# Performance work log

Hardware: AMD Instinct MI355X
Metric: run time of the kernel (lower is better)

## Reference

```python
import jax, jax.numpy as jnp
import numpy as np

N, LP, LD, D, H, GS = 16, 2048, 512, 256, 8, 4
HD = D // H           # head_size = 32
TAU = 1.0             # softmax_tau
ITERS = 4             # sinkhorn_iters
INF = 1.0e6


def setup_inputs() -> dict:
    key = jax.random.key(0)
    ks = jax.random.split(key, 10)
    inp = {
        "protein": jax.random.normal(ks[0], (N, LP, D), jnp.float32),
        "drug": jax.random.normal(ks[1], (N, LD, D), jnp.float32),
        "mask_prot": jax.random.bernoulli(ks[2], 0.9, (N, LP)),
        "mask_drug": jax.random.bernoulli(ks[3], 0.9, (N, LD)),
    }
    names = ["Wq_p", "Wk_p", "Wv_p", "Wq_d", "Wk_d", "Wv_d"]
    for i, name in enumerate(names):
        inp[name] = jax.random.normal(ks[4 + i], (D, D), jnp.float32) * (1.0 / np.sqrt(D))
    return inp


def _group(x, mask):
    n, L, d = x.shape
    g = L // GS
    xg = x.reshape(n, g, GS, d).mean(2)          # [N,G,D]
    mg = mask.reshape(n, g, GS).any(2)           # [N,G]
    return xg, mg


def _alpha_logits(logits, mask_row, mask_col):
    # logits: [N,L1,L2,H]; sinkhorn normalization as in the torch module
    n, L1, L2, h = logits.shape
    logits = logits * (1.0 / np.sqrt(HD))
    pair = mask_row[:, :, None, None] & mask_col[:, None, :, None]  # [N,L1,L2,1]
    logits = jnp.where(pair, logits, logits - INF)
    A = jax.nn.softmax((logits / TAU).reshape(n, L1 * L2, h), axis=1).reshape(n, L1, L2, h)
    valid = pair.astype(A.dtype)
    A = A * valid + 1e-12 * valid
    for _ in range(ITERS):
        row_sum = (A * valid).sum(2, keepdims=True) + 1e-12
        A = A / row_sum * valid
        col_sum = (A * valid).sum(1, keepdims=True) + 1e-12
        A = A / col_sum * valid
    return A * valid


def _proj(x, W):
    n, g, d = x.shape
    return (x @ W.T).reshape(n, g, H, HD)


def reference(protein, drug, mask_prot, mask_drug, Wq_p, Wk_p, Wv_p, Wq_d, Wk_d, Wv_d):
    pg, mp = _group(protein, mask_prot)   # [N,Gp,D], [N,Gp]
    dg, md = _group(drug, mask_drug)      # [N,Gd,D], [N,Gd]

    qp, kp, vp = _proj(pg, Wq_p), _proj(pg, Wk_p), _proj(pg, Wv_p)
    qd, kd, vd = _proj(dg, Wq_d), _proj(dg, Wk_d), _proj(dg, Wv_d)

    att = lambda q, k: jnp.einsum('blhd,bkhd->blkh', q, k)
    a_pp = _alpha_logits(att(qp, kp), mp, mp)
    a_pd = _alpha_logits(att(qp, kd), mp, md)
    a_dp = _alpha_logits(att(qd, kp), md, mp)
    a_dd = _alpha_logits(att(qd, kd), md, md)

    mix = lambda a, v: jnp.einsum('blkh,bkhd->blhd', a, v).reshape(a.shape[0], a.shape[1], D)
    prot_embedding = (mix(a_pp, vp) + mix(a_pd, vd)) * 0.5  # [N,Gp,D]
    drug_embedding = (mix(a_dp, vp) + mix(a_dd, vd)) * 0.5  # [N,Gd,D]

    # agg_mode == 'mean': masked mean over valid groups
    mpf = mp[..., None].astype(prot_embedding.dtype)
    mdf = md[..., None].astype(drug_embedding.dtype)
    prot_embed = (prot_embedding * mpf).sum(1) / mpf.sum(1)
    drug_embed = (drug_embedding * mdf).sum(1) / mdf.sum(1)

    query_embed = jnp.concatenate([prot_embed, drug_embed], axis=1)  # [N,2D]
    return query_embed, a_dp
```

## Files before the change

### kernel.cpp

```cpp
#include <hip/hip_runtime.h>
#include <hip/hip_bf16.h>

#define NB   16
#define DT   256
#define HT   8
#define HDT  32
#define GP   512
#define GD   128
#define SCL  0.17677669529663687f

using bf16x8 = __attribute__((ext_vector_type(8))) short;
using bf16x4 = __attribute__((ext_vector_type(4))) short;
using f32x4  = __attribute__((ext_vector_type(4))) float;

__device__ __forceinline__ short f2bf(float f) {
  __hip_bfloat16 h = __float2bfloat16(f);
  short s; __builtin_memcpy(&s, &h, 2);
  return s;
}

__device__ __forceinline__ bf16x8 cvt8(float4 a, float4 b) {
  bf16x8 r;
  r[0] = f2bf(a.x); r[1] = f2bf(a.y); r[2] = f2bf(a.z); r[3] = f2bf(a.w);
  r[4] = f2bf(b.x); r[5] = f2bf(b.y); r[6] = f2bf(b.z); r[7] = f2bf(b.w);
  return r;
}

extern "C" __global__ __launch_bounds__(256)
void k_group(const float* __restrict__ protein, const float* __restrict__ drug,
             const int* __restrict__ mprot, const int* __restrict__ mdrug,
             const float* __restrict__ Wk, const float* __restrict__ Wq,
             short* __restrict__ pg_bf, short* __restrict__ dg_bf,
             int* __restrict__ mp_g, int* __restrict__ md_g,
             short* __restrict__ Wk_bf, short* __restrict__ Wq_bf,
             float* __restrict__ part, int* __restrict__ cntp) {
  int b = blockIdx.x, t = threadIdx.x;
  if (b >= 640) {
    int idx = (b - 640) * 2048 + t * 8;
    const float* s; short* d;
    if (idx < 65536) { s = Wk + idx; d = Wk_bf + idx; }
    else             { s = Wq + (idx - 65536); d = Wq_bf + (idx - 65536); }
    *(bf16x8*)d = cvt8(*(const float4*)s, *(const float4*)(s + 4));
    return;
  }
  const float* src; const int* msk; short* dst; int* mg; int gbase;
  if (b < 512) { src = protein; msk = mprot; dst = pg_bf; mg = mp_g; gbase = b * 16; }
  else         { src = drug;    msk = mdrug; dst = dg_bf; mg = md_g; gbase = (b - 512) * 16; }

  __shared__ int gm_s[16];
  __shared__ float part_s[4][256];
  if (t < 16) {
    const int* m = msk + (size_t)(gbase + t) * 4;
    int v = (m[0] | m[1] | m[2] | m[3]) ? 1 : 0;
    gm_s[t] = v;
    mg[gbase + t] = v;
  }
  __syncthreads();
  if (t == 0) {
    int c = 0;
    #pragma unroll
    for (int i = 0; i < 16; ++i) c += gm_s[i];
    cntp[b] = c;
  }

  int col4 = t & 63, gsub = t >> 6;
  float a0 = 0.f, a1 = 0.f, a2 = 0.f, a3 = 0.f;
  #pragma unroll
  for (int it = 0; it < 4; ++it) {
    int grp = gbase + gsub + it * 4;
    const float* rp = src + (size_t)grp * 1024 + col4 * 4;
    float4 r0 = *(const float4*)rp;
    float4 r1 = *(const float4*)(rp + 256);
    float4 r2 = *(const float4*)(rp + 512);
    float4 r3 = *(const float4*)(rp + 768);
    float m0 = 0.25f * (r0.x + r1.x + r2.x + r3.x);
    float m1 = 0.25f * (r0.y + r1.y + r2.y + r3.y);
    float m2 = 0.25f * (r0.z + r1.z + r2.z + r3.z);
    float m3 = 0.25f * (r0.w + r1.w + r2.w + r3.w);
    bf16x4 v; v[0] = f2bf(m0); v[1] = f2bf(m1); v[2] = f2bf(m2); v[3] = f2bf(m3);
    *(bf16x4*)(dst + (size_t)grp * 256 + col4 * 4) = v;
    if (gm_s[gsub + it * 4]) { a0 += m0; a1 += m1; a2 += m2; a3 += m3; }
  }
  part_s[gsub][col4 * 4 + 0] = a0;
  part_s[gsub][col4 * 4 + 1] = a1;
  part_s[gsub][col4 * 4 + 2] = a2;
  part_s[gsub][col4 * 4 + 3] = a3;
  __syncthreads();
  part[(size_t)b * 256 + t] = part_s[0][t] + part_s[1][t] + part_s[2][t] + part_s[3][t];
}

extern "C" __global__ __launch_bounds__(256)
void k_projbf(const short* __restrict__ pg_bf, const short* __restrict__ dg_bf,
              const short* __restrict__ Wk_bf, const short* __restrict__ Wq_bf,
              short* __restrict__ kp_bf, short* __restrict__ qd_bf) {
  int b = blockIdx.x, t = threadIdx.x;
  int w = t >> 6, lane = t & 63, c15 = lane & 15, g = lane >> 4;
  const short *A, *W; short* o; int rowbase;
  if (b < 256) { A = pg_bf; W = Wk_bf; o = kp_bf; rowbase = b * 32; }
  else         { A = dg_bf; W = Wq_bf; o = qd_bf; rowbase = (b - 256) * 32; }
  int rt = rowbase + (w & 1) * 16;
  int ch = (w >> 1) * 128;

  const short* ap = A + (size_t)(rt + c15) * 256;
  f32x4 acc[8];
  #pragma unroll
  for (int i = 0; i < 8; ++i) acc[i] = (f32x4){0.f, 0.f, 0.f, 0.f};

  #pragma unroll
  for (int ks = 0; ks < 8; ++ks) {
    bf16x8 af = *(const bf16x8*)(ap + ks * 32 + g * 8);
    #pragma unroll
    for (int ct = 0; ct < 8; ++ct) {
      bf16x8 bfr = *(const bf16x8*)(W + (size_t)(ch + ct * 16 + c15) * 256 + ks * 32 + g * 8);
      acc[ct] = __builtin_amdgcn_mfma_f32_16x16x32_bf16(af, bfr, acc[ct], 0, 0, 0);
    }
  }
  #pragma unroll
  for (int ct = 0; ct < 8; ++ct) {
    #pragma unroll
    for (int r = 0; r < 4; ++r) {
      o[(size_t)(rt + 4 * g + r) * 256 + ch + ct * 16 + c15] = f2bf(acc[ct][r]);
    }
  }
}

#define FOR16(X) X(0) X(1) X(2) X(3) X(4) X(5) X(6) X(7) X(8) X(9) X(10) X(11) X(12) X(13) X(14) X(15)

extern "C" __global__ __launch_bounds__(1024)
void k_scalars(const short* __restrict__ qd, const short* __restrict__ kp,
               const int* __restrict__ md_g, const int* __restrict__ mp_g,
               float* __restrict__ rcz) {
  int bid = blockIdx.x;
  int n = ((bid & 7) << 1) | ((bid >> 3) & 1);
  int h = bid >> 4;
  int tid = threadIdx.x;
  int wid = tid >> 6, lane = tid & 63;
  int wr = wid >> 1, ch = wid & 1;
  int c15 = lane & 15, g = lane >> 4;

  __shared__ float c_s[GP];
  __shared__ float r_s[GD];
  __shared__ float t_s[GD];
  __shared__ float t2[2][GD];
  __shared__ float red[8][GP];
  __shared__ float z_sh, sr_sh, sc_sh, kv_sh;
  __shared__ int mp_sh[GP];
  __shared__ int md_sh[GD];

  if (tid < GP) { int m = mp_g[n * GP + tid]; mp_sh[tid] = m; c_s[tid] = m ? 1.f : 0.f; }
  if (tid < GD) { int m = md_g[n * GD + tid]; md_sh[tid] = m; r_s[tid] = m ? 1.f : 0.f; }
  __syncthreads();

  if (wid == 0) {
    float v = (float)(mp_sh[lane] + mp_sh[lane + 64] + mp_sh[lane + 128] + mp_sh[lane + 192] +
                      mp_sh[lane + 256] + mp_sh[lane + 320] + mp_sh[lane + 384] + mp_sh[lane + 448]);
    #pragma unroll
    for (int m = 1; m <= 32; m <<= 1) v += __shfl_xor(v, m, 64);
    if (lane == 0) kv_sh = v;
  }

  int qrow = 16 * wr + c15;
  bf16x8 af = *(const bf16x8*)(qd + ((size_t)(n * GD + qrow)) * 256 + h * HDT + g * 8);
  int row0 = 16 * wr + 4 * g;
  int mr0 = md_sh[row0], mr1 = md_sh[row0 + 1], mr2 = md_sh[row0 + 2], mr3 = md_sh[row0 + 3];
  const short* kbase = kp + ((size_t)n * GP) * 256 + h * HDT + g * 8;
  int colbase = ch * 256 + c15;

#define DECLP(i) f32x4 P##i;
  FOR16(DECLP)
#define MKP(i) { int col = colbase + 16 * (i); \
    bf16x8 bfr = *(const bf16x8*)(kbase + (size_t)col * 256); \
    f32x4 a = __builtin_amdgcn_mfma_f32_16x16x32_bf16(af, bfr, (f32x4){0.f,0.f,0.f,0.f}, 0, 0, 0); \
    int mc = mp_sh[col]; \
    P##i[0] = (mc && mr0) ? __expf(a[0] * SCL) : 0.f; \
    P##i[1] = (mc && mr1) ? __expf(a[1] * SCL) : 0.f; \
    P##i[2] = (mc && mr2) ? __expf(a[2] * SCL) : 0.f; \
    P##i[3] = (mc && mr3) ? __expf(a[3] * SCL) : 0.f; }
  FOR16(MKP)

  {
    float pa0 = 0.f, pa1 = 0.f, pa2 = 0.f, pa3 = 0.f;
#define RS0(i) pa0 += P##i[0]; pa1 += P##i[1]; pa2 += P##i[2]; pa3 += P##i[3];
    FOR16(RS0)
    #pragma unroll
    for (int m = 1; m <= 8; m <<= 1) {
      pa0 += __shfl_xor(pa0, m, 64); pa1 += __shfl_xor(pa1, m, 64);
      pa2 += __shfl_xor(pa2, m, 64); pa3 += __shfl_xor(pa3, m, 64);
    }
    if (c15 == 0) t2[ch][row0 + 0] = pa0;
    if (c15 == 1) t2[ch][row0 + 1] = pa1;
    if (c15 == 2) t2[ch][row0 + 2] = pa2;
    if (c15 == 3) t2[ch][row0 + 3] = pa3;
  }
  __syncthreads();
  if (tid < GD) t_s[tid] = t2[0][tid] + t2[1][tid];
  __syncthreads();
  if (wid == 0) {
    float v = t_s[lane] + t_s[lane + 64];
    #pragma unroll
    for (int m = 1; m <= 32; m <<= 1) v += __shfl_xor(v, m, 64);
    if (lane == 0) z_sh = v;
  }
  __syncthreads();
  float Zinv = 1.0f / z_sh;
  float Sc = kv_sh;

  #pragma unroll 1
  for (int it = 0; it < 4; ++it) {
    if (tid < GD) {
      float ti = t_s[tid] * Zinv + 1e-12f * Sc;
      float ri = r_s[tid];
      r_s[tid] = md_sh[tid] ? (ri / (ri * ti + 1e-12f)) : 0.f;
    }
    __syncthreads();
    if (wid == 0) {
      float v = r_s[lane] + r_s[lane + 64];
      #pragma unroll
      for (int m = 1; m <= 32; m <<= 1) v += __shfl_xor(v, m, 64);
      if (lane == 0) sr_sh = v;
    }
    __syncthreads();
    float Sr = sr_sh;
    {
      float rr0 = r_s[row0], rr1 = r_s[row0 + 1], rr2 = r_s[row0 + 2], rr3 = r_s[row0 + 3];
#define CP(i) { float u = P##i[0] * rr0 + P##i[1] * rr1 + P##i[2] * rr2 + P##i[3] * rr3; \
      u += __shfl_xor(u, 16, 64); u += __shfl_xor(u, 32, 64); \
      if (g == 0) red[wr][colbase + 16 * (i)] = u; }
      FOR16(CP)
    }
    __syncthreads();
    if (tid < GP) {
      float cs = red[0][tid] + red[1][tid] + red[2][tid] + red[3][tid] +
                 red[4][tid] + red[5][tid] + red[6][tid] + red[7][tid];
      float uj = cs * Zinv + 1e-12f * Sr;
      float cj = c_s[tid];
      c_s[tid] = mp_sh[tid] ? (cj / (cj * uj + 1e-12f)) : 0.f;
    }
    __syncthreads();
    if (wid == 0) {
      float v = c_s[lane] + c_s[lane + 64] + c_s[lane + 128] + c_s[lane + 192] +
                c_s[lane + 256] + c_s[lane + 320] + c_s[lane + 384] + c_s[lane + 448];
      #pragma unroll
      for (int m = 1; m <= 32; m <<= 1) v += __shfl_xor(v, m, 64);
      if (lane == 0) sc_sh = v;
    }
    __syncthreads();
    Sc = sc_sh;
    if (it < 3) {
      float qa0 = 0.f, qa1 = 0.f, qa2 = 0.f, qa3 = 0.f;
#define RP(i) { float cv = c_s[colbase + 16 * (i)]; \
      qa0 += P##i[0] * cv; qa1 += P##i[1] * cv; qa2 += P##i[2] * cv; qa3 += P##i[3] * cv; }
      FOR16(RP)
      #pragma unroll
      for (int m = 1; m <= 8; m <<= 1) {
        qa0 += __shfl_xor(qa0, m, 64); qa1 += __shfl_xor(qa1, m, 64);
        qa2 += __shfl_xor(qa2, m, 64); qa3 += __shfl_xor(qa3, m, 64);
      }
      if (c15 == 0) t2[ch][row0 + 0] = qa0;
      if (c15 == 1) t2[ch][row0 + 1] = qa1;
      if (c15 == 2) t2[ch][row0 + 2] = qa2;
      if (c15 == 3) t2[ch][row0 + 3] = qa3;
      __syncthreads();
      if (tid < GD) t_s[tid] = t2[0][tid] + t2[1][tid];
    }
  }

  size_t rb = (size_t)(n * 8 + h) * 1024;
  if (tid < GD) rcz[rb + tid] = r_s[tid];
  if (tid < GP) rcz[rb + 128 + tid] = c_s[tid];
  if (tid == 0) rcz[rb + 640] = Zinv;
}

extern "C" __global__ __launch_bounds__(256)
void k_write_embed(const short* __restrict__ qd, const short* __restrict__ kp,
                   const float* __restrict__ rcz,
                   const float* __restrict__ part, const int* __restrict__ cntp,
                   const float* __restrict__ Wvp, const float* __restrict__ Wvd,
                   float* __restrict__ out) {
  int bid = blockIdx.x;
  int t = threadIdx.x;
  if (bid >= 512) {
    int bb = bid - 512;
    int n = bb >> 3;
    int dchunk = (bb & 7) * 32;
    __shared__ float sps[256], sds[256];
    float a1 = 0.f;
    #pragma unroll
    for (int i = 0; i < 32; ++i) a1 += part[(size_t)(n * 32 + i) * 256 + t];
    sps[t] = a1;
    float a2 = 0.f;
    #pragma unroll
    for (int i = 0; i < 8; ++i) a2 += part[(size_t)(512 + n * 8 + i) * 256 + t];
    sds[t] = a2;
    __syncthreads();
    int cp = 0, cd = 0;
    #pragma unroll
    for (int i = 0; i < 32; ++i) cp += cntp[n * 32 + i];
    #pragma unroll
    for (int i = 0; i < 8; ++i) cd += cntp[512 + n * 8 + i];
    int dloc = t >> 3, ks = (t & 7) * 32;
    int d = dchunk + dloc;
    const float* wp = Wvp + (size_t)d * 256 + ks;
    const float* wd = Wvd + (size_t)d * 256 + ks;
    float acc = 0.f;
    #pragma unroll
    for (int k = 0; k < 32; k += 4) {
      float4 a = *(const float4*)(wp + k);
      float4 c = *(const float4*)(wd + k);
      acc += sps[ks + k] * a.x + sps[ks + k + 1] * a.y + sps[ks + k + 2] * a.z + sps[ks + k + 3] * a.w
           + sds[ks + k] * c.x + sds[ks + k + 1] * c.y + sds[ks + k + 2] * c.z + sds[ks + k + 3] * c.w;
    }
    #pragma unroll
    for (int m = 1; m <= 4; m <<= 1) acc += __shfl_xor(acc, m, 64);
    if ((t & 7) == 0) {
      acc *= 0.5f;
      out[n * 512 + d]       = acc / (float)cp;
      out[n * 512 + 256 + d] = acc / (float)cd;
    }
    return;
  }
  int n = ((bid & 7) << 1) | ((bid >> 3) & 1);
  int rest = bid >> 4;
  int rt = rest >> 2;
  int cc = rest & 3;
  int w = t >> 6, lane = t & 63;
  int c15 = lane & 15, g = lane >> 4;

  const short* qbase = qd + ((size_t)(n * GD + rt * 16 + c15)) * 256;
  bf16x8 af[8];
  #pragma unroll
  for (int h = 0; h < 8; ++h) af[h] = *(const bf16x8*)(qbase + h * HDT + g * 8);

  size_t rb = (size_t)n * 8 * 1024;
  float rv[8][4], zin[8];
  #pragma unroll
  for (int h = 0; h < 8; ++h) {
    const float* rp = rcz + rb + (size_t)h * 1024;
    #pragma unroll
    for (int r = 0; r < 4; ++r) rv[h][r] = rp[rt * 16 + 4 * g + r];
    zin[h] = rp[640];
  }

  #pragma unroll
  for (int ct = 0; ct < 2; ++ct) {
    int col = cc * 128 + w * 32 + ct * 16 + c15;
    f32x4 acc[8]; float cw[8];
    #pragma unroll
    for (int h = 0; h < 8; ++h) {
      bf16x8 bfr = *(const bf16x8*)(kp + ((size_t)(n * GP + col)) * 256 + h * HDT + g * 8);
      acc[h] = __builtin_amdgcn_mfma_f32_16x16x32_bf16(af[h], bfr, (f32x4){0.f,0.f,0.f,0.f}, 0, 0, 0);
      cw[h] = rcz[rb + (size_t)h * 1024 + 128 + col];
    }
    #pragma unroll
    for (int r = 0; r < 4; ++r) {
      int row = rt * 16 + 4 * g + r;
      float4 lo, hi;
      lo.x = rv[0][r] * (__expf(acc[0][r] * SCL) * zin[0] + 1e-12f) * cw[0];
      lo.y = rv[1][r] * (__expf(acc[1][r] * SCL) * zin[1] + 1e-12f) * cw[1];
      lo.z = rv[2][r] * (__expf(acc[2][r] * SCL) * zin[2] + 1e-12f) * cw[2];
      lo.w = rv[3][r] * (__expf(acc[3][r] * SCL) * zin[3] + 1e-12f) * cw[3];
      hi.x = rv[4][r] * (__expf(acc[4][r] * SCL) * zin[4] + 1e-12f) * cw[4];
      hi.y = rv[5][r] * (__expf(acc[5][r] * SCL) * zin[5] + 1e-12f) * cw[5];
      hi.z = rv[6][r] * (__expf(acc[6][r] * SCL) * zin[6] + 1e-12f) * cw[6];
      hi.w = rv[7][r] * (__expf(acc[7][r] * SCL) * zin[7] + 1e-12f) * cw[7];
      float* dst = out + 8192 + (((size_t)(n * GD + row)) * GP + col) * 8;
      *(float4*)dst = lo;
      *(float4*)(dst + 4) = hi;
    }
  }
}

extern "C" void kernel_launch(void* const* d_in, const int* in_sizes, int n_in,
                              void* d_out, int out_size, void* d_ws, size_t ws_size,
                              hipStream_t stream) {
  const float* protein = (const float*)d_in[0];
  const float* drug    = (const float*)d_in[1];
  const int*   mprot   = (const int*)d_in[2];
  const int*   mdrug   = (const int*)d_in[3];
  const float* Wk_p = (const float*)d_in[5];
  const float* Wv_p = (const float*)d_in[6];
  const float* Wq_d = (const float*)d_in[7];
  const float* Wv_d = (const float*)d_in[9];
  float* out = (float*)d_out;

  char* wsb = (char*)d_ws;
  short* pg_bf = (short*)wsb;                 wsb += (size_t)NB * GP * 256 * 2;
  short* dg_bf = (short*)wsb;                 wsb += (size_t)NB * GD * 256 * 2;
  short* kp_bf = (short*)wsb;                 wsb += (size_t)NB * GP * 256 * 2;
  short* qd_bf = (short*)wsb;                 wsb += (size_t)NB * GD * 256 * 2;
  short* Wk_bf = (short*)wsb;                 wsb += 65536 * 2;
  short* Wq_bf = (short*)wsb;                 wsb += 65536 * 2;
  float* part  = (float*)wsb;                 wsb += (size_t)640 * 256 * 4;
  float* rcz   = (float*)wsb;                 wsb += (size_t)128 * 1024 * 4;
  int*   cntp  = (int*)wsb;                   wsb += 640 * 4;
  int*   mp_g  = (int*)wsb;                   wsb += 8192 * 4;
  int*   md_g  = (int*)wsb;                   wsb += 2048 * 4;

  k_group<<<704, 256, 0, stream>>>(protein, drug, mprot, mdrug, Wk_p, Wq_d,
                                   pg_bf, dg_bf, mp_g, md_g, Wk_bf, Wq_bf,
                                   part, cntp);
  k_projbf<<<320, 256, 0, stream>>>(pg_bf, dg_bf, Wk_bf, Wq_bf, kp_bf, qd_bf);
  k_scalars<<<128, 1024, 0, stream>>>(qd_bf, kp_bf, md_g, mp_g, rcz);
  k_write_embed<<<640, 256, 0, stream>>>(qd_bf, kp_bf, rcz, part, cntp,
                                         Wv_p, Wv_d, out);
}
```

Baseline: 163.1 us.

## Move embed GEMV into projection kernel, stage K tile in LDS, trim syncs

The embedding GEMV blocks move from the final write kernel into the projection launch as 128 extra blocks, so they run alongside the projections instead of at the end. The write kernel now stages a 128-column K tile in swizzled LDS before the MFMAs, replacing repeated global loads. In the Sinkhorn kernel the exp-weight registers are stored as fp16 to cut register pressure, and block-wide scalar reductions are done redundantly per wave to remove several __syncthreads. fp16 storage of the weights lowers precision, and the 64KB LDS tile may limit occupancy of the write kernel.

```diff
diff --git a/kernel.cpp b/kernel.cpp
--- a/kernel.cpp
+++ b/kernel.cpp
@@ -12,6 +12,7 @@
 using bf16x8 = __attribute__((ext_vector_type(8))) short;
 using bf16x4 = __attribute__((ext_vector_type(4))) short;
 using f32x4  = __attribute__((ext_vector_type(4))) float;
+using h16x4  = __attribute__((ext_vector_type(4))) _Float16;
 
 __device__ __forceinline__ short f2bf(float f) {
   __hip_bfloat16 h = __float2bfloat16(f);
@@ -92,8 +93,51 @@
 extern "C" __global__ __launch_bounds__(256)
 void k_projbf(const short* __restrict__ pg_bf, const short* __restrict__ dg_bf,
               const short* __restrict__ Wk_bf, const short* __restrict__ Wq_bf,
-              short* __restrict__ kp_bf, short* __restrict__ qd_bf) {
+              short* __restrict__ kp_bf, short* __restrict__ qd_bf,
+              const float* __restrict__ part, const int* __restrict__ cntp,
+              const float* __restrict__ Wvp, const float* __restrict__ Wvd,
+              float* __restrict__ out) {
   int b = blockIdx.x, t = threadIdx.x;
+  if (b >= 320) {
+    int bb = b - 320;
+    int n = bb >> 3;
+    int dchunk = (bb & 7) * 32;
+    __shared__ float sps[256], sds[256];
+    float a1 = 0.f;
+    #pragma unroll
+    for (int i = 0; i < 32; ++i) a1 += part[(size_t)(n * 32 + i) * 256 + t];
+    sps[t] = a1;
+    float a2 = 0.f;
+    #pragma unroll
+    for (int i = 0; i < 8; ++i) a2 += part[(size_t)(512 + n * 8 + i) * 256 + t];
+    sds[t] = a2;
+    __syncthreads();
+    int cp = 0, cd = 0;
+    #pragma unroll
+    for (int i = 0; i < 32; ++i) cp += cntp[n * 32 + i];
+    #pragma unroll
+    for (int i = 0; i < 8; ++i) cd += cntp[512 + n * 8 + i];
+    int dloc = t >> 3, ks = (t & 7) * 32;
+    int d = dchunk + dloc;
+    const float* wp = Wvp + (size_t)d * 256 + ks;
+    const float* wd = Wvd + (size_t)d * 256 + ks;
+    float acc = 0.f;
+    #pragma unroll
+    for (int k = 0; k < 32; k += 4) {
+      float4 a = *(const float4*)(wp + k);
+      float4 c = *(const float4*)(wd + k);
+      acc += sps[ks + k] * a.x + sps[ks + k + 1] * a.y + sps[ks + k + 2] * a.z + sps[ks + k + 3] * a.w
+           + sds[ks + k] * c.x + sds[ks + k + 1] * c.y + sds[ks + k + 2] * c.z + sds[ks + k + 3] * c.w;
+    }
+    #pragma unroll
+    for (int m = 1; m <= 4; m <<= 1) acc += __shfl_xor(acc, m, 64);
+    if ((t & 7) == 0) {
+      acc *= 0.5f;
+      out[n * 512 + d]       = acc / (float)cp;
+      out[n * 512 + 256 + d] = acc / (float)cd;
+    }
+    return;
+  }
   int w = t >> 6, lane = t & 63, c15 = lane & 15, g = lane >> 4;
   const short *A, *W; short* o; int rowbase;
   if (b < 256) { A = pg_bf; W = Wk_bf; o = kp_bf; rowbase = b * 32; }
@@ -140,10 +184,8 @@
 
   __shared__ float c_s[GP];
   __shared__ float r_s[GD];
-  __shared__ float t_s[GD];
   __shared__ float t2[2][GD];
   __shared__ float red[8][GP];
-  __shared__ float z_sh, sr_sh, sc_sh, kv_sh;
   __shared__ int mp_sh[GP];
   __shared__ int md_sh[GD];
 
@@ -151,12 +193,13 @@
   if (tid < GD) { int m = md_g[n * GD + tid]; md_sh[tid] = m; r_s[tid] = m ? 1.f : 0.f; }
   __syncthreads();
 
-  if (wid == 0) {
+  float kv;
+  {
     float v = (float)(mp_sh[lane] + mp_sh[lane + 64] + mp_sh[lane + 128] + mp_sh[lane + 192] +
                       mp_sh[lane + 256] + mp_sh[lane + 320] + mp_sh[lane + 384] + mp_sh[lane + 448]);
     #pragma unroll
     for (int m = 1; m <= 32; m <<= 1) v += __shfl_xor(v, m, 64);
-    if (lane == 0) kv_sh = v;
+    kv = v;
   }
 
   int qrow = 16 * wr + c15;
@@ -166,21 +209,21 @@
   const short* kbase = kp + ((size_t)n * GP) * 256 + h * HDT + g * 8;
   int colbase = ch * 256 + c15;
 
-#define DECLP(i) f32x4 P##i;
+#define DECLP(i) h16x4 P##i;
   FOR16(DECLP)
 #define MKP(i) { int col = colbase + 16 * (i); \
     bf16x8 bfr = *(const bf16x8*)(kbase + (size_t)col * 256); \
     f32x4 a = __builtin_amdgcn_mfma_f32_16x16x32_bf16(af, bfr, (f32x4){0.f,0.f,0.f,0.f}, 0, 0, 0); \
     int mc = mp_sh[col]; \
-    P##i[0] = (mc && mr0) ? __expf(a[0] * SCL) : 0.f; \
-    P##i[1] = (mc && mr1) ? __expf(a[1] * SCL) : 0.f; \
-    P##i[2] = (mc && mr2) ? __expf(a[2] * SCL) : 0.f; \
-    P##i[3] = (mc && mr3) ? __expf(a[3] * SCL) : 0.f; }
+    P##i[0] = (_Float16)((mc && mr0) ? __expf(a[0] * SCL) : 0.f); \
+    P##i[1] = (_Float16)((mc && mr1) ? __expf(a[1] * SCL) : 0.f); \
+    P##i[2] = (_Float16)((mc && mr2) ? __expf(a[2] * SCL) : 0.f); \
+    P##i[3] = (_Float16)((mc && mr3) ? __expf(a[3] * SCL) : 0.f); }
   FOR16(MKP)
 
   {
     float pa0 = 0.f, pa1 = 0.f, pa2 = 0.f, pa3 = 0.f;
-#define RS0(i) pa0 += P##i[0]; pa1 += P##i[1]; pa2 += P##i[2]; pa3 += P##i[3];
+#define RS0(i) pa0 += (float)P##i[0]; pa1 += (float)P##i[1]; pa2 += (float)P##i[2]; pa3 += (float)P##i[3];
     FOR16(RS0)
     #pragma unroll
     for (int m = 1; m <= 8; m <<= 1) {
@@ -193,37 +236,34 @@
     if (c15 == 3) t2[ch][row0 + 3] = pa3;
   }
   __syncthreads();
-  if (tid < GD) t_s[tid] = t2[0][tid] + t2[1][tid];
-  __syncthreads();
-  if (wid == 0) {
-    float v = t_s[lane] + t_s[lane + 64];
+  float Zinv;
+  {
+    float v = t2[0][lane] + t2[1][lane] + t2[0][lane + 64] + t2[1][lane + 64];
     #pragma unroll
     for (int m = 1; m <= 32; m <<= 1) v += __shfl_xor(v, m, 64);
-    if (lane == 0) z_sh = v;
-  }
-  __syncthreads();
-  float Zinv = 1.0f / z_sh;
-  float Sc = kv_sh;
+    Zinv = 1.0f / v;
+  }
+  float Sc = kv;
 
   #pragma unroll 1
   for (int it = 0; it < 4; ++it) {
     if (tid < GD) {
-      float ti = t_s[tid] * Zinv + 1e-12f * Sc;
+      float ti = (t2[0][tid] + t2[1][tid]) * Zinv + 1e-12f * Sc;
       float ri = r_s[tid];
       r_s[tid] = md_sh[tid] ? (ri / (ri * ti + 1e-12f)) : 0.f;
     }
     __syncthreads();
-    if (wid == 0) {
+    float Sr;
+    {
       float v = r_s[lane] + r_s[lane + 64];
       #pragma unroll
       for (int m = 1; m <= 32; m <<= 1) v += __shfl_xor(v, m, 64);
-      if (lane == 0) sr_sh = v;
-    }
-    __syncthreads();
-    float Sr = sr_sh;
+      Sr = v;
+    }
     {
       float rr0 = r_s[row0], rr1 = r_s[row0 + 1], rr2 = r_s[row0 + 2], rr3 = r_s[row0 + 3];
-#define CP(i) { float u = P##i[0] * rr0 + P##i[1] * rr1 + P##i[2] * rr2 + P##i[3] * rr3; \
+#define CP(i) { float u = (float)P##i[0] * rr0 + (float)P##i[1] * rr1 + \
+                         (float)P##i[2] * rr2 + (float)P##i[3] * rr3; \
       u += __shfl_xor(u, 16, 64); u += __shfl_xor(u, 32, 64); \
       if (g == 0) red[wr][colbase + 16 * (i)] = u; }
       FOR16(CP)
@@ -237,19 +277,18 @@
       c_s[tid] = mp_sh[tid] ? (cj / (cj * uj + 1e-12f)) : 0.f;
     }
     __syncthreads();
-    if (wid == 0) {
-      float v = c_s[lane] + c_s[lane + 64] + c_s[lane + 128] + c_s[lane + 192] +
-                c_s[lane + 256] + c_s[lane + 320] + c_s[lane + 384] + c_s[lane + 448];
-      #pragma unroll
-      for (int m = 1; m <= 32; m <<= 1) v += __shfl_xor(v, m, 64);
-      if (lane == 0) sc_sh = v;
-    }
-    __syncthreads();
-    Sc = sc_sh;
     if (it < 3) {
+      {
+        float v = c_s[lane] + c_s[lane + 64] + c_s[lane + 128] + c_s[lane + 192] +
+                  c_s[lane + 256] + c_s[lane + 320] + c_s[lane + 384] + c_s[lane + 448];
+        #pragma unroll
+        for (int m = 1; m <= 32; m <<= 1) v += __shfl_xor(v, m, 64);
+        Sc = v;
+      }
       float qa0 = 0.f, qa1 = 0.f, qa2 = 0.f, qa3 = 0.f;
 #define RP(i) { float cv = c_s[colbase + 16 * (i)]; \
-      qa0 += P##i[0] * cv; qa1 += P##i[1] * cv; qa2 += P##i[2] * cv; qa3 += P##i[3] * cv; }
+      qa0 += (float)P##i[0] * cv; qa1 += (float)P##i[1] * cv; \
+      qa2 += (float)P##i[2] * cv; qa3 += (float)P##i[3] * cv; }
       FOR16(RP)
       #pragma unroll
       for (int m = 1; m <= 8; m <<= 1) {
@@ -261,7 +300,6 @@
       if (c15 == 2) t2[ch][row0 + 2] = qa2;
       if (c15 == 3) t2[ch][row0 + 3] = qa3;
       __syncthreads();
-      if (tid < GD) t_s[tid] = t2[0][tid] + t2[1][tid];
     }
   }
 
@@ -272,60 +310,28 @@
 }
 
 extern "C" __global__ __launch_bounds__(256)
-void k_write_embed(const short* __restrict__ qd, const short* __restrict__ kp,
-                   const float* __restrict__ rcz,
-                   const float* __restrict__ part, const int* __restrict__ cntp,
-                   const float* __restrict__ Wvp, const float* __restrict__ Wvd,
-                   float* __restrict__ out) {
+void k_write(const short* __restrict__ qd, const short* __restrict__ kp,
+             const float* __restrict__ rcz, float* __restrict__ out) {
   int bid = blockIdx.x;
-  int t = threadIdx.x;
-  if (bid >= 512) {
-    int bb = bid - 512;
-    int n = bb >> 3;
-    int dchunk = (bb & 7) * 32;
-    __shared__ float sps[256], sds[256];
-    float a1 = 0.f;
-    #pragma unroll
-    for (int i = 0; i < 32; ++i) a1 += part[(size_t)(n * 32 + i) * 256 + t];
-    sps[t] = a1;
-    float a2 = 0.f;
-    #pragma unroll
-    for (int i = 0; i < 8; ++i) a2 += part[(size_t)(512 + n * 8 + i) * 256 + t];
-    sds[t] = a2;
-    __syncthreads();
-    int cp = 0, cd = 0;
-    #pragma unroll
-    for (int i = 0; i < 32; ++i) cp += cntp[n * 32 + i];
-    #pragma unroll
-    for (int i = 0; i < 8; ++i) cd += cntp[512 + n * 8 + i];
-    int dloc = t >> 3, ks = (t & 7) * 32;
-    int d = dchunk + dloc;
-    const float* wp = Wvp + (size_t)d * 256 + ks;
-    const float* wd = Wvd + (size_t)d * 256 + ks;
-    float acc = 0.f;
-    #pragma unroll
-    for (int k = 0; k < 32; k += 4) {
-      float4 a = *(const float4*)(wp + k);
-      float4 c = *(const float4*)(wd + k);
-      acc += sps[ks + k] * a.x + sps[ks + k + 1] * a.y + sps[ks + k + 2] * a.z + sps[ks + k + 3] * a.w
-           + sds[ks + k] * c.x + sds[ks + k + 1] * c.y + sds[ks + k + 2] * c.z + sds[ks + k + 3] * c.w;
-    }
-    #pragma unroll
-    for (int m = 1; m <= 4; m <<= 1) acc += __shfl_xor(acc, m, 64);
-    if ((t & 7) == 0) {
-      acc *= 0.5f;
-      out[n * 512 + d]       = acc / (float)cp;
-      out[n * 512 + 256 + d] = acc / (float)cd;
-    }
-    return;
-  }
   int n = ((bid & 7) << 1) | ((bid >> 3) & 1);
   int rest = bid >> 4;
   int rt = rest >> 2;
   int cc = rest & 3;
+  int t = threadIdx.x;
   int w = t >> 6, lane = t & 63;
   int c15 = lane & 15, g = lane >> 4;
 
+  __shared__ short ktile[32768];
+
+  const short* kpsrc = kp + ((size_t)(n * GP + cc * 128)) * 256;
+  #pragma unroll
+  for (int j = 0; j < 16; ++j) {
+    int flatb = j * 4096 + t * 16;
+    int col = flatb >> 9, db = flatb & 511;
+    bf16x8 v = *(const bf16x8*)(kpsrc + ((size_t)col << 8) + (db >> 1));
+    *(bf16x8*)&ktile[(col * 512 + (db ^ ((col & 7) << 4))) >> 1] = v;
+  }
+
   const short* qbase = qd + ((size_t)(n * GD + rt * 16 + c15)) * 256;
   bf16x8 af[8];
   #pragma unroll
@@ -340,14 +346,17 @@
     for (int r = 0; r < 4; ++r) rv[h][r] = rp[rt * 16 + 4 * g + r];
     zin[h] = rp[640];
   }
+  __syncthreads();
 
   #pragma unroll
   for (int ct = 0; ct < 2; ++ct) {
-    int col = cc * 128 + w * 32 + ct * 16 + c15;
+    int lc = w * 32 + ct * 16 + c15;
+    int col = cc * 128 + lc;
     f32x4 acc[8]; float cw[8];
     #pragma unroll
     for (int h = 0; h < 8; ++h) {
-      bf16x8 bfr = *(const bf16x8*)(kp + ((size_t)(n * GP + col)) * 256 + h * HDT + g * 8);
+      int db = (h * 64 + g * 16) ^ ((lc & 7) << 4);
+      bf16x8 bfr = *(const bf16x8*)&ktile[(lc * 512 + db) >> 1];
       acc[h] = __builtin_amdgcn_mfma_f32_16x16x32_bf16(af[h], bfr, (f32x4){0.f,0.f,0.f,0.f}, 0, 0, 0);
       cw[h] = rcz[rb + (size_t)h * 1024 + 128 + col];
     }
@@ -399,8 +408,8 @@
   k_group<<<704, 256, 0, stream>>>(protein, drug, mprot, mdrug, Wk_p, Wq_d,
                                    pg_bf, dg_bf, mp_g, md_g, Wk_bf, Wq_bf,
                                    part, cntp);
-  k_projbf<<<320, 256, 0, stream>>>(pg_bf, dg_bf, Wk_bf, Wq_bf, kp_bf, qd_bf);
+  k_projbf<<<448, 256, 0, stream>>>(pg_bf, dg_bf, Wk_bf, Wq_bf, kp_bf, qd_bf,
+                                    part, cntp, Wv_p, Wv_d, out);
   k_scalars<<<128, 1024, 0, stream>>>(qd_bf, kp_bf, md_g, mp_g, rcz);
-  k_write_embed<<<640, 256, 0, stream>>>(qd_bf, kp_bf, rcz, part, cntp,
-                                         Wv_p, Wv_d, out);
-}
+  k_write<<<512, 256, 0, stream>>>(qd_bf, kp_bf, rcz, out);
+}
```

Result: faster. 158.7 us (-2.7%).
